# Optimization experiments

Hardware: AMD Instinct MI355X
Metric: run time of the kernel (lower is better)

## Reference

```python
import jax, jax.numpy as jnp
import numpy as np

B, T, D, H = 2, 2048, 1024, 16
HS = D // H  # per-head size = head_size//num_heads with head_size=D
EPS = 1e-5


def layer_norm(x, g, b):
    mu = jnp.mean(x, axis=-1, keepdims=True)
    var = jnp.mean((x - mu) ** 2, axis=-1, keepdims=True)
    return (x - mu) * jax.lax.rsqrt(var + EPS) * g + b


def setup_inputs() -> dict:
    key = jax.random.key(0)
    ks = jax.random.split(key, 12)
    s = lambda n: 1.0 / np.sqrt(n)
    return {
        "x": jax.random.normal(ks[0], (B, T, D), dtype=jnp.float32),
        "Wq": jax.random.normal(ks[1], (H, D, HS), dtype=jnp.float32) * s(D),
        "Wk": jax.random.normal(ks[2], (H, D, HS), dtype=jnp.float32) * s(D),
        "Wv": jax.random.normal(ks[3], (H, D, HS), dtype=jnp.float32) * s(D),
        "Wproj": jax.random.normal(ks[4], (D, D), dtype=jnp.float32) * s(D),
        "bproj": jnp.zeros((D,), dtype=jnp.float32),
        "W1": jax.random.normal(ks[5], (D, 4 * D), dtype=jnp.float32) * s(D),
        "b1": jnp.zeros((4 * D,), dtype=jnp.float32),
        "W2": jax.random.normal(ks[6], (4 * D, D), dtype=jnp.float32) * s(4 * D),
        "b2": jnp.zeros((D,), dtype=jnp.float32),
        "ln1_g": jnp.ones((D,), dtype=jnp.float32),
        "ln1_b": jnp.zeros((D,), dtype=jnp.float32),
        "ln2_g": jnp.ones((D,), dtype=jnp.float32),
        "ln2_b": jnp.zeros((D,), dtype=jnp.float32),
    }


def reference(x, Wq, Wk, Wv, Wproj, bproj, W1, b1, W2, b2, ln1_g, ln1_b, ln2_g, ln2_b):
    # x = LN1(x); x = x + sa(x)  (residual uses normalized x, per source)
    xn = layer_norm(x, ln1_g, ln1_b)
    q = jnp.einsum("btd,hde->bhte", xn, Wq)  # [B,H,T,HS]
    k = jnp.einsum("btd,hde->bhte", xn, Wk)
    v = jnp.einsum("btd,hde->bhte", xn, Wv)
    # scale uses C = embedding dim (not head size), per source
    scores = jnp.einsum("bhqe,bhke->bhqk", q, k) * (D ** -0.5)
    mask = jnp.tril(jnp.ones((T, T), dtype=bool))  # [Tq,Tk]
    scores = jnp.where(mask, scores, -jnp.inf)
    # softmax over dim=1 of [B,T,T] in source => QUERY axis (axis=2 here)
    w = jax.nn.softmax(scores, axis=2)
    attn = jnp.einsum("bhqk,bhke->bhqe", w, v)  # [B,H,T,HS]
    attn = attn.transpose(0, 2, 1, 3).reshape(B, T, D)
    sa = attn @ Wproj + bproj
    x1 = xn + sa
    # x = LN2(x); x = x + ffwd(x)
    x1n = layer_norm(x1, ln2_g, ln2_b)
    h = jax.nn.relu(x1n @ W1 + b1)
    ff = h @ W2 + b2
    return x1n + ff
```

## Files before the change

### kernel.cpp

```cpp
#include <hip/hip_runtime.h>
#include <math.h>

#define B_ 2
#define T_ 2048
#define D_ 1024
#define H_ 16
#define HS_ 64
#define BT_ (B_*T_)
#define EPS_ 1e-5f
#define SCALE_ 0.03125f
#define C2_ (0.03125f * 1.44269504088896f)

typedef __attribute__((ext_vector_type(4))) float f32x4;
typedef __attribute__((ext_vector_type(8))) __bf16 bf16x8;

__device__ __forceinline__ short f2bf(float f) {
    union { float f; unsigned u; } cv; cv.f = f;
    unsigned u = cv.u;
    return (short)((u + 0x7fffu + ((u >> 16) & 1u)) >> 16);
}

__global__ __launch_bounds__(256) void ln_kernel(const float* __restrict__ x,
        const float* __restrict__ g, const float* __restrict__ b,
        float* __restrict__ out, short* __restrict__ outb) {
    int row = blockIdx.x;
    int tid = threadIdx.x;
    const float* xr = x + (size_t)row * D_;
    float4 v = *(const float4*)(xr + tid * 4);
    __shared__ float red[256];
    red[tid] = v.x + v.y + v.z + v.w;
    __syncthreads();
    for (int st = 128; st > 0; st >>= 1) {
        if (tid < st) red[tid] += red[tid + st];
        __syncthreads();
    }
    float mean = red[0] * (1.0f / D_);
    __syncthreads();
    float dx = v.x - mean, dy = v.y - mean, dz = v.z - mean, dw = v.w - mean;
    red[tid] = dx*dx + dy*dy + dz*dz + dw*dw;
    __syncthreads();
    for (int st = 128; st > 0; st >>= 1) {
        if (tid < st) red[tid] += red[tid + st];
        __syncthreads();
    }
    float rstd = rsqrtf(red[0] * (1.0f / D_) + EPS_);
    float4 gv = *(const float4*)(g + tid * 4);
    float4 bv = *(const float4*)(b + tid * 4);
    float4 o;
    o.x = dx * rstd * gv.x + bv.x;
    o.y = dy * rstd * gv.y + bv.y;
    o.z = dz * rstd * gv.z + bv.z;
    o.w = dw * rstd * gv.w + bv.w;
    *(float4*)(out + (size_t)row * D_ + tid * 4) = o;
    short4 ob = make_short4(f2bf(o.x), f2bf(o.y), f2bf(o.z), f2bf(o.w));
    *(short4*)(outb + (size_t)row * D_ + tid * 4) = ob;
}

__global__ __launch_bounds__(256) void transpose_cvt(const float* __restrict__ in,
        short* __restrict__ out, int R, int C) {
    __shared__ float t[32][33];
    int c0 = blockIdx.x * 32, r0 = blockIdx.y * 32;
    const float* inb = in + (size_t)blockIdx.z * R * C;
    short* outb = out + (size_t)blockIdx.z * R * C;
    int tx = threadIdx.x & 31, ty = threadIdx.x >> 5;
    #pragma unroll
    for (int i = 0; i < 32; i += 8)
        t[ty + i][tx] = inb[(size_t)(r0 + ty + i) * C + c0 + tx];
    __syncthreads();
    #pragma unroll
    for (int i = 0; i < 32; i += 8)
        outb[(size_t)(c0 + ty + i) * R + r0 + tx] = f2bf(t[tx][ty + i]);
}

__global__ __launch_bounds__(256) void gemm_qkv(
        const short* __restrict__ A, const short* __restrict__ Bt,
        short* __restrict__ qo, short* __restrict__ ko, short* __restrict__ vo,
        int M, int N, int K) {
    __shared__ char As[2][16384];
    __shared__ char Bs[2][16384];
    int tid = threadIdx.x;
    int lane = tid & 63, w = tid >> 6;
    int wr = w >> 1, wc = w & 1;

    int orig = blockIdx.y * gridDim.x + blockIdx.x;
    int cpx = (gridDim.x * gridDim.y) >> 3;
    int wgid = (orig & 7) * cpx + (orig >> 3);
    int m0 = (wgid / gridDim.x) * 128;
    int n0 = (wgid % gridDim.x) * 128;

    f32x4 acc[4][4] = {};

    int rowS[4], kbS[4];
    #pragma unroll
    for (int i = 0; i < 4; ++i) {
        int o = (w * 4 + i) * 1024 + lane * 16;
        rowS[i] = o >> 7;
        kbS[i] = (o & 127) ^ ((rowS[i] & 7) << 4);
    }
    const size_t Kb = (size_t)K * 2;

    #define STAGE_G(buf, kt) do {                                              \
        _Pragma("unroll")                                                      \
        for (int i_ = 0; i_ < 4; ++i_) {                                       \
            int c_ = w * 4 + i_;                                               \
            const char* ga_ = (const char*)A + (size_t)(m0 + rowS[i_]) * Kb    \
                              + (size_t)(kt) * 2 + kbS[i_];                    \
            __builtin_amdgcn_global_load_lds(                                  \
                (const __attribute__((address_space(1))) void*)ga_,            \
                (__attribute__((address_space(3))) void*)(As[buf] + c_ * 1024),\
                16, 0, 0);                                                     \
            const char* gb_ = (const char*)Bt + (size_t)(n0 + rowS[i_]) * Kb   \
                              + (size_t)(kt) * 2 + kbS[i_];                    \
            __builtin_amdgcn_global_load_lds(                                  \
                (const __attribute__((address_space(1))) void*)gb_,            \
                (__attribute__((address_space(3))) void*)(Bs[buf] + c_ * 1024),\
                16, 0, 0);                                                     \
        }                                                                      \
    } while (0)

    int nt = K >> 6;
    STAGE_G(0, 0);
    for (int t = 0; t < nt; ++t) {
        int cur = t & 1;
        if (t + 1 < nt) {
            STAGE_G(cur ^ 1, (t + 1) * 64);
            asm volatile("s_waitcnt vmcnt(8)" ::: "memory");
        } else {
            asm volatile("s_waitcnt vmcnt(0)" ::: "memory");
        }
        __builtin_amdgcn_s_barrier();
        __builtin_amdgcn_s_setprio(1);
        #pragma unroll
        for (int kk = 0; kk < 2; ++kk) {
            int kbyte = kk * 64 + (lane >> 4) * 16;
            bf16x8 af[4], bf[4];
            #pragma unroll
            for (int mi = 0; mi < 4; ++mi) {
                int row = wr * 64 + mi * 16 + (lane & 15);
                af[mi] = *(const bf16x8*)(As[cur] + row * 128 + (kbyte ^ ((row & 7) << 4)));
            }
            #pragma unroll
            for (int ni = 0; ni < 4; ++ni) {
                int row = wc * 64 + ni * 16 + (lane & 15);
                bf[ni] = *(const bf16x8*)(Bs[cur] + row * 128 + (kbyte ^ ((row & 7) << 4)));
            }
            #pragma unroll
            for (int mi = 0; mi < 4; ++mi)
                #pragma unroll
                for (int ni = 0; ni < 4; ++ni)
                    acc[mi][ni] = __builtin_amdgcn_mfma_f32_16x16x32_bf16(
                        af[mi], bf[ni], acc[mi][ni], 0, 0, 0);
        }
        __builtin_amdgcn_s_setprio(0);
        __builtin_amdgcn_s_barrier();
    }
    #undef STAGE_G

    #pragma unroll
    for (int mi = 0; mi < 4; ++mi) {
        #pragma unroll
        for (int j = 0; j < 4; ++j) {
            int row = m0 + wr * 64 + mi * 16 + (lane >> 4) * 4 + j;
            #pragma unroll
            for (int ni = 0; ni < 4; ++ni) {
                int col = n0 + wc * 64 + ni * 16 + (lane & 15);
                float vv = acc[mi][ni][j];
                int sel = col >> 10, rem = col & 1023;
                int h = rem >> 6, e = rem & 63;
                int bb = row >> 11, tt = row & 2047;
                short bv = f2bf(vv);
                if (sel == 0)
                    qo[(((size_t)(bb * H_ + h)) * T_ + tt) * HS_ + e] = bv;
                else if (sel == 1)
                    ko[(((size_t)(bb * H_ + h)) * T_ + tt) * HS_ + e] = bv;
                else
                    vo[(((size_t)(bb * H_ + h)) * HS_ + e) * T_ + tt] = bv;
            }
        }
    }
}

template<bool BIAS, bool RES, bool RELU, bool BF16OUT>
__global__ __launch_bounds__(256) void gemm_12864(
        const short* __restrict__ A, const short* __restrict__ Bt,
        const float* __restrict__ bias, const float* __restrict__ res,
        float* __restrict__ C, short* __restrict__ Cb,
        int M, int N, int K) {
    __shared__ char As[2][16384];
    __shared__ char Bs[2][8192];
    int tid = threadIdx.x, lane = tid & 63, w = tid >> 6;

    int orig = blockIdx.y * gridDim.x + blockIdx.x;
    int cpx = (gridDim.x * gridDim.y) >> 3;
    int wgid = (orig & 7) * cpx + (orig >> 3);
    int m0 = (wgid / gridDim.x) * 128;
    int n0 = (wgid % gridDim.x) * 64;

    const size_t Kb = (size_t)K * 2;
    int rowA[4], cbA[4], rowB[2], cbB[2];
    #pragma unroll
    for (int i = 0; i < 4; ++i) {
        int o = (w * 4 + i) * 1024 + lane * 16;
        rowA[i] = o >> 7;
        cbA[i] = (o & 127) ^ ((rowA[i] & 7) << 4);
    }
    #pragma unroll
    for (int i = 0; i < 2; ++i) {
        int o = (w * 2 + i) * 1024 + lane * 16;
        rowB[i] = o >> 7;
        cbB[i] = (o & 127) ^ ((rowB[i] & 7) << 4);
    }

    #define STAGE_S(buf, kt) do {                                              \
        _Pragma("unroll")                                                      \
        for (int i_ = 0; i_ < 4; ++i_) {                                       \
            const char* ga_ = (const char*)A + (size_t)(m0 + rowA[i_]) * Kb    \
                              + (size_t)(kt) * 2 + cbA[i_];                    \
            __builtin_amdgcn_global_load_lds(                                  \
                (const __attribute__((address_space(1))) void*)ga_,            \
                (__attribute__((address_space(3))) void*)(As[buf] + (w * 4 + i_) * 1024),\
                16, 0, 0);                                                     \
        }                                                                      \
        _Pragma("unroll")                                                      \
        for (int i_ = 0; i_ < 2; ++i_) {                                       \
            const char* gb_ = (const char*)Bt + (size_t)(n0 + rowB[i_]) * Kb   \
                              + (size_t)(kt) * 2 + cbB[i_];                    \
            __builtin_amdgcn_global_load_lds(                                  \
                (const __attribute__((address_space(1))) void*)gb_,            \
                (__attribute__((address_space(3))) void*)(Bs[buf] + (w * 2 + i_) * 1024),\
                16, 0, 0);                                                     \
        }                                                                      \
    } while (0)

    f32x4 acc[2][4] = {};
    int nt = K >> 6;
    STAGE_S(0, 0);
    for (int t = 0; t < nt; ++t) {
        int cur = t & 1;
        if (t + 1 < nt) {
            STAGE_S(cur ^ 1, (t + 1) * 64);
            asm volatile("s_waitcnt vmcnt(6)" ::: "memory");
        } else {
            asm volatile("s_waitcnt vmcnt(0)" ::: "memory");
        }
        __builtin_amdgcn_s_barrier();
        __builtin_amdgcn_s_setprio(1);
        #pragma unroll
        for (int kk = 0; kk < 2; ++kk) {
            int kbyte = kk * 64 + (lane >> 4) * 16;
            bf16x8 bf[4], af[2];
            #pragma unroll
            for (int ni = 0; ni < 4; ++ni) {
                int row = ni * 16 + (lane & 15);
                bf[ni] = *(const bf16x8*)(Bs[cur] + row * 128 + (kbyte ^ ((row & 7) << 4)));
            }
            #pragma unroll
            for (int mi = 0; mi < 2; ++mi) {
                int row = w * 32 + mi * 16 + (lane & 15);
                af[mi] = *(const bf16x8*)(As[cur] + row * 128 + (kbyte ^ ((row & 7) << 4)));
            }
            #pragma unroll
            for (int mi = 0; mi < 2; ++mi)
                #pragma unroll
                for (int ni = 0; ni < 4; ++ni)
                    acc[mi][ni] = __builtin_amdgcn_mfma_f32_16x16x32_bf16(
                        af[mi], bf[ni], acc[mi][ni], 0, 0, 0);
        }
        __builtin_amdgcn_s_setprio(0);
        __builtin_amdgcn_s_barrier();
    }
    #undef STAGE_S

    #pragma unroll
    for (int mi = 0; mi < 2; ++mi) {
        #pragma unroll
        for (int j = 0; j < 4; ++j) {
            int row = m0 + w * 32 + mi * 16 + (lane >> 4) * 4 + j;
            #pragma unroll
            for (int ni = 0; ni < 4; ++ni) {
                int col = n0 + ni * 16 + (lane & 15);
                float vv = acc[mi][ni][j];
                if (BIAS) vv += bias[col];
                if (RES)  vv += res[(size_t)row * N + col];
                if (RELU) vv = fmaxf(vv, 0.0f);
                if (BF16OUT) Cb[(size_t)row * N + col] = f2bf(vv);
                else         C[(size_t)row * N + col] = vv;
            }
        }
    }
}

template<bool BIAS, bool RELU, bool BF16OUT>
__global__ __launch_bounds__(512, 2) void gemm256_2p(
        const short* __restrict__ A, const short* __restrict__ Bt,
        const float* __restrict__ bias,
        float* __restrict__ C, short* __restrict__ Cb,
        int M, int N, int K) {
    __shared__ char As[2][32768];
    __shared__ char Bs[2][32768];
    int tid = threadIdx.x, lane = tid & 63, w = tid >> 6;
    int wr = w >> 2, wc = w & 3;

    int nwg = gridDim.x * gridDim.y;
    int orig = blockIdx.y * gridDim.x + blockIdx.x;
    int cpx = nwg >> 3;
    int wgid = (orig & 7) * cpx + (orig >> 3);
    int m0 = (wgid / gridDim.x) * 256;
    int n0 = (wgid % gridDim.x) * 256;

    const size_t Kb = (size_t)K * 2;
    int rowS[4], cbS[4];
    #pragma unroll
    for (int i = 0; i < 4; ++i) {
        int o = (i * 8 + w) * 1024 + lane * 16;
        rowS[i] = o >> 7;
        cbS[i] = (o & 127) ^ ((rowS[i] & 7) << 4);
    }

    #define STAGE_256(buf, kt) do {                                           \
        _Pragma("unroll")                                                     \
        for (int i_ = 0; i_ < 4; ++i_) {                                      \
            int c_ = i_ * 8 + w;                                              \
            const char* ga_ = (const char*)A + (size_t)(m0 + rowS[i_]) * Kb   \
                              + (size_t)(kt) * 2 + cbS[i_];                   \
            __builtin_amdgcn_global_load_lds(                                 \
                (const __attribute__((address_space(1))) void*)ga_,           \
                (__attribute__((address_space(3))) void*)(As[buf] + c_ * 1024),\
                16, 0, 0);                                                    \
            const char* gb_ = (const char*)Bt + (size_t)(n0 + rowS[i_]) * Kb  \
                              + (size_t)(kt) * 2 + cbS[i_];                   \
            __builtin_amdgcn_global_load_lds(                                 \
                (const __attribute__((address_space(1))) void*)gb_,           \
                (__attribute__((address_space(3))) void*)(Bs[buf] + c_ * 1024),\
                16, 0, 0);                                                    \
        }                                                                     \
    } while (0)

    f32x4 acc[8][4] = {};
    int nt = K >> 6;
    STAGE_256(0, 0);
    for (int t = 0; t < nt; ++t) {
        int cur = t & 1;
        if (t + 1 < nt) {
            STAGE_256(cur ^ 1, (t + 1) * 64);
            asm volatile("s_waitcnt vmcnt(8)" ::: "memory");
        } else {
            asm volatile("s_waitcnt vmcnt(0)" ::: "memory");
        }
        __builtin_amdgcn_s_barrier();
        __builtin_amdgcn_s_setprio(1);
        #pragma unroll
        for (int kk = 0; kk < 2; ++kk) {
            int kbyte = kk * 64 + (lane >> 4) * 16;
            bf16x8 bfr[4];
            #pragma unroll
            for (int ni = 0; ni < 4; ++ni) {
                int row = wc * 64 + ni * 16 + (lane & 15);
                bfr[ni] = *(const bf16x8*)(Bs[cur] + row * 128 + (kbyte ^ ((row & 7) << 4)));
            }
            #pragma unroll
            for (int mi = 0; mi < 8; ++mi) {
                int row = wr * 128 + mi * 16 + (lane & 15);
                bf16x8 afr = *(const bf16x8*)(As[cur] + row * 128 + (kbyte ^ ((row & 7) << 4)));
                #pragma unroll
                for (int ni = 0; ni < 4; ++ni)
                    acc[mi][ni] = __builtin_amdgcn_mfma_f32_16x16x32_bf16(
                        afr, bfr[ni], acc[mi][ni], 0, 0, 0);
            }
        }
        __builtin_amdgcn_s_setprio(0);
        __builtin_amdgcn_s_barrier();
    }
    #undef STAGE_256

    #pragma unroll
    for (int mi = 0; mi < 8; ++mi) {
        #pragma unroll
        for (int j = 0; j < 4; ++j) {
            int row = m0 + wr * 128 + mi * 16 + (lane >> 4) * 4 + j;
            #pragma unroll
            for (int ni = 0; ni < 4; ++ni) {
                int col = n0 + wc * 64 + ni * 16 + (lane & 15);
                float vv = acc[mi][ni][j];
                if (BIAS) vv += bias[col];
                if (RELU) vv = fmaxf(vv, 0.0f);
                if (BF16OUT) Cb[(size_t)row * N + col] = f2bf(vv);
                else         C[(size_t)row * N + col] = vv;
            }
        }
    }
}

__global__ __launch_bounds__(256) void attn_pass1_mfma(
        const short* __restrict__ qg, const short* __restrict__ kg,
        float* __restrict__ lpart) {
    int kt = blockIdx.x;
    int chunk = blockIdx.y;
    int bh = blockIdx.z;
    int tid = threadIdx.x, lane = tid & 63, w = tid >> 6;
    __shared__ char Qs[8192];
    const size_t base = (size_t)bh * T_ * HS_;
    int kb0 = kt * 128;
    bf16x8 af[2][2];
    #pragma unroll
    for (int s2 = 0; s2 < 2; ++s2) {
        const short* kr = kg + base
            + (size_t)(kb0 + s2 * 64 + w * 16 + (lane & 15)) * HS_ + (lane >> 4) * 8;
        af[s2][0] = *(const bf16x8*)kr;
        af[s2][1] = *(const bf16x8*)(kr + 32);
    }
    int baseT = kt * 2;
    int R = 32 - baseT;
    int cnt = (R + 3) >> 2;
    int qs = baseT + chunk * cnt;
    int qe = qs + cnt; if (qe > 32) qe = 32;
    float psum[2][4] = {};
    for (int qt = qs; qt < qe; ++qt) {
        __syncthreads();
        #pragma unroll
        for (int it = 0; it < 2; ++it) {
            int o = it * 4096 + w * 1024 + lane * 16;
            int row = o >> 7;
            int col = (o & 127) ^ ((row & 7) << 4);
            const char* src = (const char*)(qg + base + (size_t)(qt * 64 + row) * HS_) + col;
            __builtin_amdgcn_global_load_lds(
                (const __attribute__((address_space(1))) void*)src,
                (__attribute__((address_space(3))) void*)(Qs + it * 4096 + w * 1024), 16, 0, 0);
        }
        __syncthreads();
        #pragma unroll
        for (int sub = 0; sub < 4; ++sub) {
            int qrow = sub * 16 + (lane & 15);
            bf16x8 bq[2];
            #pragma unroll
            for (int kk = 0; kk < 2; ++kk) {
                int off = (kk * 64 + (lane >> 4) * 16) ^ ((qrow & 7) << 4);
                bq[kk] = *(const bf16x8*)(Qs + qrow * 128 + off);
            }
            int qglob = qt * 64 + qrow;
            #pragma unroll
            for (int s2 = 0; s2 < 2; ++s2) {
                f32x4 c = {0.f, 0.f, 0.f, 0.f};
                c = __builtin_amdgcn_mfma_f32_16x16x32_bf16(af[s2][0], bq[0], c, 0, 0, 0);
                c = __builtin_amdgcn_mfma_f32_16x16x32_bf16(af[s2][1], bq[1], c, 0, 0, 0);
                #pragma unroll
                for (int j = 0; j < 4; ++j) {
                    int kglob = kb0 + s2 * 64 + w * 16 + (lane >> 4) * 4 + j;
                    float pe = exp2f(c[j] * C2_);
                    psum[s2][j] += (qglob >= kglob) ? pe : 0.0f;
                }
            }
        }
    }
    #pragma unroll
    for (int s2 = 0; s2 < 2; ++s2)
        #pragma unroll
        for (int j = 0; j < 4; ++j) {
            float v = psum[s2][j];
            v += __shfl_xor(v, 1); v += __shfl_xor(v, 2);
            v += __shfl_xor(v, 4); v += __shfl_xor(v, 8);
            psum[s2][j] = v;
        }
    if ((lane & 15) == 0) {
        #pragma unroll
        for (int s2 = 0; s2 < 2; ++s2)
            #pragma unroll
            for (int j = 0; j < 4; ++j)
                lpart[((size_t)chunk * 32 + bh) * T_
                      + kb0 + s2 * 64 + w * 16 + (lane >> 4) * 4 + j] = psum[s2][j];
    }
}

__global__ __launch_bounds__(256) void lreduce(const float* __restrict__ lpart,
        float* __restrict__ rl) {
    int i = blockIdx.x * 256 + threadIdx.x;
    const int S = 32 * T_;
    float s = lpart[i] + lpart[S + i] + lpart[2 * S + i] + lpart[3 * S + i];
    rl[i] = -log2f(s);
}

__global__ __launch_bounds__(256) void attn_pass2_mfma(
        const short* __restrict__ qg, const short* __restrict__ kg,
        const short* __restrict__ vt, const float* __restrict__ rl,
        short* __restrict__ attnb) {
    int pair = blockIdx.x, bh = blockIdx.y;
    int bb = bh >> 4, hh = bh & 15;
    int tid = threadIdx.x, lane = tid & 63, w = tid >> 6;
    __shared__ char Kb[2][16384];
    __shared__ char Vb[2][16384];
    __shared__ char Ps[8192];
    __shared__ float rlds[2][128];
    const size_t qkbase = (size_t)bh * T_ * HS_;
    const size_t vtbase = (size_t)bh * HS_ * T_;

    #pragma unroll 1
    for (int half = 0; half < 2; ++half) {
        int qtile = half == 0 ? pair : 31 - pair;
        int q0 = qtile * 64 + w * 16;
        bf16x8 aq[2];
        {
            const short* qr = qg + qkbase + (size_t)(q0 + (lane & 15)) * HS_ + (lane >> 4) * 8;
            aq[0] = *(const bf16x8*)qr;
            aq[1] = *(const bf16x8*)(qr + 32);
        }
        f32x4 oacc[4] = {};
        int nkeys = qtile * 64 + 64;
        int nstep = (nkeys + 127) >> 7;

        #define STAGE_P2(bufi, stepi) do {                                        \
            int k0_ = (stepi) * 128;                                              \
            _Pragma("unroll")                                                     \
            for (int i_ = 0; i_ < 4; ++i_) {                                      \
                int c_ = w * 4 + i_;                                              \
                int o_ = c_ * 1024 + lane * 16;                                   \
                int krow_ = o_ >> 7;                                              \
                int kcol_ = (o_ & 127) ^ ((krow_ & 7) << 4);                      \
                const char* srcK_ = (const char*)(kg + qkbase                     \
                    + (size_t)(k0_ + krow_) * HS_) + kcol_;                       \
                __builtin_amdgcn_global_load_lds(                                 \
                    (const __attribute__((address_space(1))) void*)srcK_,         \
                    (__attribute__((address_space(3))) void*)(Kb[bufi] + c_ * 1024), \
                    16, 0, 0);                                                    \
                int vrow_ = o_ >> 8;                                              \
                int vcol_ = (o_ & 255) ^ ((vrow_ & 7) << 4);                      \
                const char* srcV_ = (const char*)(vt + vtbase                     \
                    + (size_t)vrow_ * T_ + (size_t)k0_) + vcol_;                  \
                __builtin_amdgcn_global_load_lds(                                 \
                    (const __attribute__((address_space(1))) void*)srcV_,         \
                    (__attribute__((address_space(3))) void*)(Vb[bufi] + c_ * 1024), \
                    16, 0, 0);                                                    \
            }                                                                     \
            if (tid < 128) rlds[bufi][tid] = rl[(size_t)bh * T_ + k0_ + tid];     \
        } while (0)

        STAGE_P2(0, 0);
        __syncthreads();
        for (int st = 0; st < nstep; ++st) {
            int cur = st & 1;
            if (st + 1 < nstep) STAGE_P2(cur ^ 1, st + 1);
            #pragma unroll
            for (int sub64 = 0; sub64 < 2; ++sub64) {
                int k64 = st * 2 + sub64;
                int kbase = k64 * 64;
                if (kbase >= nkeys) break;
                bool diag = (k64 == qtile);
                const char* Ks = Kb[cur] + sub64 * 8192;
                int qgl = q0 + (lane & 15);
                int ql = w * 16 + (lane & 15);
                int swz = (ql & 7) << 4;
                #pragma unroll
                for (int sub = 0; sub < 4; ++sub) {
                    int krow = sub * 16 + (lane & 15);
                    f32x4 c = {0.f, 0.f, 0.f, 0.f};
                    #pragma unroll
                    for (int kk = 0; kk < 2; ++kk) {
                        int off = (kk * 64 + (lane >> 4) * 16) ^ ((krow & 7) << 4);
                        bf16x8 bk = *(const bf16x8*)(Ks + krow * 128 + off);
                        c = __builtin_amdgcn_mfma_f32_16x16x32_bf16(bk, aq[kk], c, 0, 0, 0);
                    }
                    int kloc0 = sub * 16 + (lane >> 4) * 4;
                    f32x4 lg4 = *(const f32x4*)&rlds[cur][sub64 * 64 + kloc0];
                    float wv[4];
                    #pragma unroll
                    for (int j = 0; j < 4; ++j) {
                        float t = exp2f(fmaf(c[j], C2_, lg4[j]));
                        int keyg = kbase + kloc0 + j;
                        wv[j] = (diag && qgl < keyg) ? 0.0f : t;
                    }
                    unsigned p01, p23;
                    asm("v_cvt_pk_bf16_f32 %0, %1, %2" : "=v"(p01) : "v"(wv[0]), "v"(wv[1]));
                    asm("v_cvt_pk_bf16_f32 %0, %1, %2" : "=v"(p23) : "v"(wv[2]), "v"(wv[3]));
                    *(unsigned*)(Ps + ql * 128 + ((kloc0 * 2) ^ swz)) = p01;
                    *(unsigned*)(Ps + ql * 128 + ((kloc0 * 2 + 4) ^ swz)) = p23;
                }
                bf16x8 ap[2];
                #pragma unroll
                for (int kk = 0; kk < 2; ++kk) {
                    int off = (kk * 64 + (lane >> 4) * 16) ^ swz;
                    ap[kk] = *(const bf16x8*)(Ps + ql * 128 + off);
                }
                #pragma unroll
                for (int es = 0; es < 4; ++es) {
                    int erow = es * 16 + (lane & 15);
                    #pragma unroll
                    for (int kk = 0; kk < 2; ++kk) {
                        int vcol = (sub64 * 128 + kk * 64 + (lane >> 4) * 16) ^ ((erow & 7) << 4);
                        bf16x8 bv = *(const bf16x8*)(Vb[cur] + erow * 256 + vcol);
                        oacc[es] = __builtin_amdgcn_mfma_f32_16x16x32_bf16(ap[kk], bv, oacc[es], 0, 0, 0);
                    }
                }
            }
            __syncthreads();
        }
        #undef STAGE_P2
        #pragma unroll
        for (int es = 0; es < 4; ++es) {
            #pragma unroll
            for (int j = 0; j < 4; ++j) {
                int qgl = q0 + (lane >> 4) * 4 + j;
                int e = es * 16 + (lane & 15);
                attnb[((size_t)(bb * T_ + qgl)) * D_ + hh * HS_ + e] = f2bf(oacc[es][j]);
            }
        }
        __syncthreads();
    }
}

extern "C" void kernel_launch(void* const* d_in, const int* in_sizes, int n_in,
                              void* d_out, int out_size, void* d_ws, size_t ws_size,
                              hipStream_t stream) {
    const float* x     = (const float*)d_in[0];
    const float* Wq    = (const float*)d_in[1];
    const float* Wk    = (const float*)d_in[2];
    const float* Wv    = (const float*)d_in[3];
    const float* Wproj = (const float*)d_in[4];
    const float* bproj = (const float*)d_in[5];
    const float* W1    = (const float*)d_in[6];
    const float* b1    = (const float*)d_in[7];
    const float* W2    = (const float*)d_in[8];
    const float* b2    = (const float*)d_in[9];
    const float* ln1g  = (const float*)d_in[10];
    const float* ln1b  = (const float*)d_in[11];
    const float* ln2g  = (const float*)d_in[12];
    const float* ln2b  = (const float*)d_in[13];
    float* out = (float*)d_out;

    const size_t MB = 1u << 20;
    char* ws = (char*)d_ws;
    float* xn    = (float*)(ws + 0 * MB);
    short* xnb   = (short*)(ws + 16 * MB);
    short* qbh   = (short*)(ws + 24 * MB);
    short* kbh   = (short*)(ws + 32 * MB);
    short* vtb   = (short*)(ws + 40 * MB);
    short* attnb = (short*)(ws + 48 * MB);
    float* x1    = (float*)(ws + 56 * MB);
    float* x1n   = (float*)(ws + 72 * MB);
    short* x1nb  = (short*)(ws + 88 * MB);
    short* hb    = (short*)(ws + 96 * MB);
    short* wqkv  = (short*)(ws + 128 * MB);
    short* wprjt = (short*)(ws + 134 * MB);
    short* w1t   = (short*)(ws + 136 * MB);
    short* w2t   = (short*)(ws + 144 * MB);
    float* lpart = (float*)(ws + 152 * MB);
    float* rl    = (float*)(ws + 153 * MB);

    transpose_cvt<<<dim3(2, 32, 16), 256, 0, stream>>>(Wq, wqkv + (size_t)0 * 1048576, 1024, 64);
    transpose_cvt<<<dim3(2, 32, 16), 256, 0, stream>>>(Wk, wqkv + (size_t)1 * 1048576, 1024, 64);
    transpose_cvt<<<dim3(2, 32, 16), 256, 0, stream>>>(Wv, wqkv + (size_t)2 * 1048576, 1024, 64);
    transpose_cvt<<<dim3(32, 32, 1), 256, 0, stream>>>(Wproj, wprjt, 1024, 1024);
    transpose_cvt<<<dim3(128, 32, 1), 256, 0, stream>>>(W1, w1t, 1024, 4096);
    transpose_cvt<<<dim3(32, 128, 1), 256, 0, stream>>>(W2, w2t, 4096, 1024);

    ln_kernel<<<dim3(BT_), 256, 0, stream>>>(x, ln1g, ln1b, xn, xnb);
    gemm_qkv<<<dim3(24, 32), 256, 0, stream>>>(
        xnb, wqkv, qbh, kbh, vtb, BT_, 3072, 1024);
    attn_pass1_mfma<<<dim3(16, 4, 32), 256, 0, stream>>>(qbh, kbh, lpart);
    lreduce<<<dim3(32 * T_ / 256), 256, 0, stream>>>(lpart, rl);
    attn_pass2_mfma<<<dim3(16, 32), 256, 0, stream>>>(qbh, kbh, vtb, rl, attnb);
    gemm_12864<true, true, false, false><<<dim3(16, 32), 256, 0, stream>>>(
        attnb, wprjt, bproj, xn, x1, nullptr, BT_, 1024, 1024);
    ln_kernel<<<dim3(BT_), 256, 0, stream>>>(x1, ln2g, ln2b, x1n, x1nb);
    gemm256_2p<true, true, true><<<dim3(16, 16), 512, 0, stream>>>(
        x1nb, w1t, b1, nullptr, hb, BT_, 4096, 1024);
    gemm_12864<true, true, false, false><<<dim3(16, 32), 256, 0, stream>>>(
        hb, w2t, b2, x1n, out, nullptr, BT_, 1024, 4096);
    (void)in_sizes; (void)n_in; (void)out_size; (void)ws_size;
}
```

Measured before the change: 312.3 us.

## Use split-K 128x128 tile GEMM with separate reduction for FFN down projection

Replaces the final FFN down-projection GEMM (K=4096) with a 128x128-tile kernel that splits K into two halves across grid z. Each half writes fp32 partials into reused workspace, and a separate elementwise kernel sums them with bias and residual. The goal is higher per-block data reuse from larger tiles while keeping enough blocks, at the cost of extra partial-result memory traffic and one more launch.

```diff
diff --git a/kernel.cpp b/kernel.cpp
--- a/kernel.cpp
+++ b/kernel.cpp
@@ -178,6 +178,121 @@
             }
         }
     }
+}
+
+__global__ __launch_bounds__(256) void gemm128_sk(
+        const short* __restrict__ A, const short* __restrict__ Bt,
+        float* __restrict__ P, int M, int N, int Ksl, int Ktot) {
+    __shared__ char As[2][16384];
+    __shared__ char Bs[2][16384];
+    int tid = threadIdx.x;
+    int lane = tid & 63, w = tid >> 6;
+    int wr = w >> 1, wc = w & 1;
+
+    int orig = blockIdx.y * gridDim.x + blockIdx.x;
+    int cpx = (gridDim.x * gridDim.y) >> 3;
+    int wgid = (orig & 7) * cpx + (orig >> 3);
+    int m0 = (wgid / gridDim.x) * 128;
+    int n0 = (wgid % gridDim.x) * 128;
+    int k0 = blockIdx.z * Ksl;
+    float* Pz = P + (size_t)blockIdx.z * M * N;
+
+    f32x4 acc[4][4] = {};
+
+    int rowS[4], kbS[4];
+    #pragma unroll
+    for (int i = 0; i < 4; ++i) {
+        int o = (w * 4 + i) * 1024 + lane * 16;
+        rowS[i] = o >> 7;
+        kbS[i] = (o & 127) ^ ((rowS[i] & 7) << 4);
+    }
+    const size_t Kb = (size_t)Ktot * 2;
+
+    #define STAGE_K(buf, kt) do {                                              \
+        _Pragma("unroll")                                                      \
+        for (int i_ = 0; i_ < 4; ++i_) {                                       \
+            int c_ = w * 4 + i_;                                               \
+            const char* ga_ = (const char*)A + (size_t)(m0 + rowS[i_]) * Kb    \
+                              + (size_t)(k0 + (kt)) * 2 + kbS[i_];             \
+            __builtin_amdgcn_global_load_lds(                                  \
+                (const __attribute__((address_space(1))) void*)ga_,            \
+                (__attribute__((address_space(3))) void*)(As[buf] + c_ * 1024),\
+                16, 0, 0);                                                     \
+            const char* gb_ = (const char*)Bt + (size_t)(n0 + rowS[i_]) * Kb   \
+                              + (size_t)(k0 + (kt)) * 2 + kbS[i_];             \
+            __builtin_amdgcn_global_load_lds(                                  \
+                (const __attribute__((address_space(1))) void*)gb_,            \
+                (__attribute__((address_space(3))) void*)(Bs[buf] + c_ * 1024),\
+                16, 0, 0);                                                     \
+        }                                                                      \
+    } while (0)
+
+    int nt = Ksl >> 6;
+    STAGE_K(0, 0);
+    for (int t = 0; t < nt; ++t) {
+        int cur = t & 1;
+        if (t + 1 < nt) {
+            STAGE_K(cur ^ 1, (t + 1) * 64);
+            asm volatile("s_waitcnt vmcnt(8)" ::: "memory");
+        } else {
+            asm volatile("s_waitcnt vmcnt(0)" ::: "memory");
+        }
+        __builtin_amdgcn_s_barrier();
+        __builtin_amdgcn_s_setprio(1);
+        #pragma unroll
+        for (int kk = 0; kk < 2; ++kk) {
+            int kbyte = kk * 64 + (lane >> 4) * 16;
+            bf16x8 af[4], bf[4];
+            #pragma unroll
+            for (int mi = 0; mi < 4; ++mi) {
+                int row = wr * 64 + mi * 16 + (lane & 15);
+                af[mi] = *(const bf16x8*)(As[cur] + row * 128 + (kbyte ^ ((row & 7) << 4)));
+            }
+            #pragma unroll
+            for (int ni = 0; ni < 4; ++ni) {
+                int row = wc * 64 + ni * 16 + (lane & 15);
+                bf[ni] = *(const bf16x8*)(Bs[cur] + row * 128 + (kbyte ^ ((row & 7) << 4)));
+            }
+            #pragma unroll
+            for (int mi = 0; mi < 4; ++mi)
+                #pragma unroll
+                for (int ni = 0; ni < 4; ++ni)
+                    acc[mi][ni] = __builtin_amdgcn_mfma_f32_16x16x32_bf16(
+                        af[mi], bf[ni], acc[mi][ni], 0, 0, 0);
+        }
+        __builtin_amdgcn_s_setprio(0);
+        __builtin_amdgcn_s_barrier();
+    }
+    #undef STAGE_K
+
+    #pragma unroll
+    for (int mi = 0; mi < 4; ++mi) {
+        #pragma unroll
+        for (int j = 0; j < 4; ++j) {
+            int row = m0 + wr * 64 + mi * 16 + (lane >> 4) * 4 + j;
+            #pragma unroll
+            for (int ni = 0; ni < 4; ++ni) {
+                int col = n0 + wc * 64 + ni * 16 + (lane & 15);
+                Pz[(size_t)row * N + col] = acc[mi][ni][j];
+            }
+        }
+    }
+}
+
+__global__ __launch_bounds__(256) void addreduce(const float* __restrict__ p0,
+        const float* __restrict__ p1, const float* __restrict__ bias,
+        const float* __restrict__ res, float* __restrict__ out) {
+    int i = blockIdx.x * 256 + threadIdx.x;
+    float4 a = ((const float4*)p0)[i];
+    float4 b = ((const float4*)p1)[i];
+    float4 r = ((const float4*)res)[i];
+    float4 bs = ((const float4*)bias)[i & 255];
+    float4 o;
+    o.x = a.x + b.x + r.x + bs.x;
+    o.y = a.y + b.y + r.y + bs.y;
+    o.z = a.z + b.z + r.z + bs.z;
+    o.w = a.w + b.w + r.w + bs.w;
+    ((float4*)out)[i] = o;
 }
 
 template<bool BIAS, bool RES, bool RELU, bool BF16OUT>
@@ -643,6 +758,9 @@
     short* w2t   = (short*)(ws + 144 * MB);
     float* lpart = (float*)(ws + 152 * MB);
     float* rl    = (float*)(ws + 153 * MB);
+    float* partP = (float*)(ws + 0 * MB);
+    float* part0 = (float*)(ws + 0 * MB);
+    float* part1 = (float*)(ws + 16 * MB);
 
     transpose_cvt<<<dim3(2, 32, 16), 256, 0, stream>>>(Wq, wqkv + (size_t)0 * 1048576, 1024, 64);
     transpose_cvt<<<dim3(2, 32, 16), 256, 0, stream>>>(Wk, wqkv + (size_t)1 * 1048576, 1024, 64);
@@ -662,7 +780,9 @@
     ln_kernel<<<dim3(BT_), 256, 0, stream>>>(x1, ln2g, ln2b, x1n, x1nb);
     gemm256_2p<true, true, true><<<dim3(16, 16), 512, 0, stream>>>(
         x1nb, w1t, b1, nullptr, hb, BT_, 4096, 1024);
-    gemm_12864<true, true, false, false><<<dim3(16, 32), 256, 0, stream>>>(
-        hb, w2t, b2, x1n, out, nullptr, BT_, 1024, 4096);
+    gemm128_sk<<<dim3(8, 32, 2), 256, 0, stream>>>(
+        hb, w2t, partP, BT_, 1024, 2048, 4096);
+    addreduce<<<dim3(BT_ * D_ / 4 / 256), 256, 0, stream>>>(
+        part0, part1, b2, x1n, out);
     (void)in_sizes; (void)n_in; (void)out_size; (void)ws_size;
 }
```

Result: no change. 307.9 us (-1.4%).
